# Optimization experiments

Measured on AMD Instinct MI355X. Metric: run time of the kernel, lower is better.

Reference implementation:

```python
import jax, jax.numpy as jnp
import numpy as np

H = 256
EDGE_DIM = 16
B, N = 8, 4096
E = 524288
EPS = 1e-5


def setup_inputs() -> dict:
    key = jax.random.key(0)
    ks = jax.random.split(key, 16)
    s = 0.02
    return {
        "h": jax.random.normal(ks[0], (B, N, H), dtype=jnp.float32),
        "edge_index": jax.random.randint(ks[1], (2, E), 0, B * N, dtype=jnp.int64),
        "edge_attr": jax.random.normal(ks[2], (E, EDGE_DIM), dtype=jnp.float32),
        "mask": jnp.ones((B, N), dtype=jnp.float32),
        # message_net params
        "W1": jax.random.normal(ks[3], (2 * H + EDGE_DIM, H), dtype=jnp.float32) * s,
        "b1": jnp.zeros((H,), dtype=jnp.float32),
        "W2": jax.random.normal(ks[4], (H, H), dtype=jnp.float32) * s,
        "b2": jnp.zeros((H,), dtype=jnp.float32),
        # update_net params
        "U1": jax.random.normal(ks[5], (2 * H, H), dtype=jnp.float32) * s,
        "c1": jnp.zeros((H,), dtype=jnp.float32),
        "U2": jax.random.normal(ks[6], (H, H), dtype=jnp.float32) * s,
        "c2": jnp.zeros((H,), dtype=jnp.float32),
        # LayerNorm params
        "gamma": jnp.ones((H,), dtype=jnp.float32),
        "beta": jnp.zeros((H,), dtype=jnp.float32),
    }


def reference(h, edge_index, edge_attr, mask, W1, b1, W2, b2, U1, c1, U2, c2, gamma, beta):
    batch, n_nodes, hid = h.shape
    h_flat = h.reshape(-1, hid)                       # (B*N, H)
    src, dst = edge_index[0], edge_index[1]
    # gather -> message MLP
    msg_in = jnp.concatenate([h_flat[src], h_flat[dst], edge_attr], axis=-1)  # (E, 2H+16)
    messages = jax.nn.silu(msg_in @ W1 + b1) @ W2 + b2                        # (E, H)
    # scatter-add aggregation by destination node
    aggr = jax.ops.segment_sum(messages, dst, num_segments=batch * n_nodes)   # (B*N, H)
    # update MLP + residual (dropout = identity in eval mode)
    upd_in = jnp.concatenate([h_flat, aggr], axis=-1)                         # (B*N, 2H)
    h_new = h_flat + (jax.nn.silu(upd_in @ U1 + c1) @ U2 + c2)
    # LayerNorm over last dim
    mu = jnp.mean(h_new, axis=-1, keepdims=True)
    var = jnp.mean(jnp.square(h_new - mu), axis=-1, keepdims=True)
    h_new = (h_new - mu) * jax.lax.rsqrt(var + EPS) * gamma + beta
    return h_new.reshape(batch, n_nodes, hid) * mask[..., None]
```

## Files before the change

kernel.cpp:

```cpp
#include <hip/hip_runtime.h>

#define H_DIM 256
#define E_NUM 524288
#define NN    32768
#define K2    512
#define K2S   520
#define SAS   264
#define XS    264

typedef unsigned short u16;
typedef unsigned int   u32;
typedef __attribute__((ext_vector_type(8))) short s16x8;
typedef __attribute__((ext_vector_type(4))) float f32x4;
typedef __attribute__((ext_vector_type(2))) float f32x2;
typedef __attribute__((ext_vector_type(4))) unsigned short u16x4;

__device__ __forceinline__ u16 f2b(float x) {
    u32 u = __float_as_uint(x);
    u32 r = (u + 0x7FFFu + ((u >> 16) & 1u)) >> 16;
    return (u16)r;
}
__device__ __forceinline__ float b2f(u16 v) {
    u32 u = ((u32)v) << 16;
    return __uint_as_float(u);
}
__device__ __forceinline__ float fsig(float x) {
    return __builtin_amdgcn_rcpf(1.f + __expf(-x));
}

__global__ __launch_bounds__(256) void k_prep_w(
    const float* __restrict__ W1, const float* __restrict__ W2,
    const float* __restrict__ U1, const float* __restrict__ U2,
    u16* __restrict__ WpqT, u16* __restrict__ W2T,
    u16* __restrict__ U1T, u16* __restrict__ U2T) {
    int idx = blockIdx.x * 256 + threadIdx.x;
    if (idx < 131072) {
        int c = idx >> 8, k = idx & 255;
        float v = (c < 256) ? W1[k * 256 + c] : W1[(256 + k) * 256 + (c - 256)];
        WpqT[idx] = f2b(v);
    } else if (idx < 196608) {
        int i = idx - 131072; int c = i >> 8, k = i & 255;
        W2T[i] = f2b(W2[k * 256 + c]);
    } else if (idx < 327680) {
        int i = idx - 196608; int c = i >> 9, k = i & 511;
        U1T[i] = f2b(U1[(size_t)k * 256 + c]);
    } else if (idx < 393216) {
        int i = idx - 327680; int c = i >> 8, k = i & 255;
        U2T[i] = f2b(U2[k * 256 + c]);
    }
}

__global__ __launch_bounds__(256) void k_hist(const int* __restrict__ eidx,
                                              int* __restrict__ cnt) {
    int i = blockIdx.x * 256 + threadIdx.x;
    if (i < E_NUM) atomicAdd(&cnt[eidx[E_NUM + i]], 1);
}

__global__ __launch_bounds__(256) void k_scan(const int* __restrict__ cnt,
                                              int* __restrict__ base,
                                              int* __restrict__ nxt) {
    __shared__ int wsum[4];
    const int t = threadIdx.x, lane = t & 63, w = t >> 6;
    const int st = t * 128;
    int s = 0;
#pragma unroll 8
    for (int i = 0; i < 128; ++i) s += cnt[st + i];
    int sc = s;
#pragma unroll
    for (int off = 1; off < 64; off <<= 1) {
        int v = __shfl_up(sc, off);
        if (lane >= off) sc += v;
    }
    if (lane == 63) wsum[w] = sc;
    __syncthreads();
    int woff = 0;
    for (int i = 0; i < w; ++i) woff += wsum[i];
    const int excl = woff + sc - s;
    if (t == 255) base[NN] = woff + sc;
    int off = excl;
    for (int i = 0; i < 128; ++i) {
        int v = cnt[st + i];
        base[st + i] = off;
        nxt[st + i] = off;
        off += v;
    }
}

__global__ __launch_bounds__(256) void k_scatter(const int* __restrict__ eidx,
                                                 int* __restrict__ nxt,
                                                 int* __restrict__ elist,
                                                 float* __restrict__ eas,
                                                 const float* __restrict__ ea) {
    int i = blockIdx.x * 256 + threadIdx.x;
    if (i < E_NUM) {
        int d = eidx[E_NUM + i];
        int p = atomicAdd(&nxt[d], 1);
        elist[p] = eidx[i];
        const float4* s = reinterpret_cast<const float4*>(ea + (size_t)i * 16);
        float4* o = reinterpret_cast<float4*>(eas + (size_t)p * 16);
        float4 v0 = s[0], v1 = s[1], v2 = s[2], v3 = s[3];
        o[0] = v0; o[1] = v1; o[2] = v2; o[3] = v3;
    }
}

__global__ __launch_bounds__(256, 2) void k_gemm_pq(
    const float* __restrict__ h, const u16* __restrict__ WpqT,
    u16* __restrict__ PQ) {
    __shared__ __align__(16) u16 sA[64 * SAS];
    const int t = threadIdx.x;
    const int n0 = blockIdx.x * 64;
    {
        const int r = t >> 2, g = t & 3;
        const float* hrow = h + (size_t)(n0 + r) * 256;
        u16* rowp = sA + r * SAS;
#pragma unroll
        for (int j = 0; j < 8; ++j) {
            const int c = g + 4 * j;
            float4 v0 = *reinterpret_cast<const float4*>(hrow + c * 8);
            float4 v1 = *reinterpret_cast<const float4*>(hrow + c * 8 + 4);
            s16x8 o;
            o[0] = (short)f2b(v0.x); o[1] = (short)f2b(v0.y);
            o[2] = (short)f2b(v0.z); o[3] = (short)f2b(v0.w);
            o[4] = (short)f2b(v1.x); o[5] = (short)f2b(v1.y);
            o[6] = (short)f2b(v1.z); o[7] = (short)f2b(v1.w);
            *reinterpret_cast<s16x8*>(rowp + c * 8) = o;
        }
    }
    __syncthreads();
    const int lane = t & 63, wv = t >> 6;
    const int l15 = lane & 15, l4 = lane >> 4;
    const int colBase = wv * 64 + l15;
    const f32x4 z4 = {0.f, 0.f, 0.f, 0.f};

    for (int q = 0; q < 2; ++q) {
        f32x4 acc[4][4];
#pragma unroll
        for (int m = 0; m < 4; ++m)
#pragma unroll
            for (int n = 0; n < 4; ++n) acc[m][n] = z4;
        const u16* Bb = WpqT + (size_t)(q * 256 + colBase) * 256 + l4 * 8;
        for (int kk = 0; kk < 8; ++kk) {
            s16x8 a[4], b[4];
#pragma unroll
            for (int m = 0; m < 4; ++m)
                a[m] = *reinterpret_cast<const s16x8*>(sA + (m * 16 + l15) * SAS + kk * 32 + l4 * 8);
#pragma unroll
            for (int n = 0; n < 4; ++n)
                b[n] = *reinterpret_cast<const s16x8*>(Bb + (size_t)n * 16 * 256 + kk * 32);
#pragma unroll
            for (int m = 0; m < 4; ++m)
#pragma unroll
                for (int n = 0; n < 4; ++n)
                    acc[m][n] = __builtin_amdgcn_mfma_f32_16x16x32_bf16(a[m], b[n], acc[m][n], 0, 0, 0);
        }
#pragma unroll
        for (int m = 0; m < 4; ++m)
#pragma unroll
            for (int j = 0; j < 4; ++j) {
                const int row = n0 + m * 16 + l4 * 4 + j;
                u16* op = PQ + (size_t)row * 512 + q * 256 + colBase;
#pragma unroll
                for (int n = 0; n < 4; ++n) op[n * 16] = f2b(acc[m][n][j]);
            }
    }
}


#define LDEA(S0, S1, S2, S3, k) do {                                        \
    const float* _ep = eas + (size_t)(eBeg + cb + min((k), m - 1)) * 16;    \
    S0 = *reinterpret_cast<const float4*>(_ep);                             \
    S1 = *reinterpret_cast<const float4*>(_ep + 4);                         \
    S2 = *reinterpret_cast<const float4*>(_ep + 8);                         \
    S3 = *reinterpret_cast<const float4*>(_ep + 12);                        \
} while (0)

__global__ __launch_bounds__(256, 4) void k_aggr(
    const u16* __restrict__ PQ, const int* __restrict__ elist,
    const int* __restrict__ base, const float* __restrict__ eas,
    const float* __restrict__ W1, const float* __restrict__ b1,
    u16* __restrict__ Sb) {
    const int t = threadIdx.x, lane = t & 63, wv = t >> 6;
    const int c0 = lane * 4;
    f32x2 WrL[16], WrH[16];
#pragma unroll
    for (int k = 0; k < 16; ++k) {
        float4 w = *reinterpret_cast<const float4*>(W1 + (size_t)(512 + k) * 256 + c0);
        WrL[k] = f32x2{w.x, w.y};
        WrH[k] = f32x2{w.z, w.w};
    }
    const float4 b1v = *reinterpret_cast<const float4*>(b1 + c0);

    const int d = __builtin_amdgcn_readfirstlane(blockIdx.x * 4 + wv);
    f32x2 qbL = {b1v.x, b1v.y}, qbH = {b1v.z, b1v.w};
    {
        u16x4 qv = *reinterpret_cast<const u16x4*>(PQ + (size_t)d * 512 + 256 + c0);
        qbL[0] += b2f(qv.x); qbL[1] += b2f(qv.y);
        qbH[0] += b2f(qv.z); qbH[1] += b2f(qv.w);
    }
    const int eBeg = __builtin_amdgcn_readfirstlane(base[d]);
    const int nAll = __builtin_amdgcn_readfirstlane(base[d + 1]) - eBeg;
    f32x2 accL = {0.f, 0.f}, accH = {0.f, 0.f};

    for (int cb = 0; cb < nAll; cb += 64) {
        const int m = min(64, nAll - cb);
        const int eeX = elist[eBeg + cb + min(lane, m - 1)];

        auto gather = [&](int idx) -> u16x4 {
            const int s = __builtin_amdgcn_readlane(eeX, idx);
            return *reinterpret_cast<const u16x4*>(PQ + (size_t)s * 512 + c0);
        };
        auto edge_compute = [&](const u16x4& pc, const float4& E0, const float4& E1,
                                const float4& E2, const float4& E3) {
            f32x2 xL = qbL, xH = qbH;
            xL[0] += b2f(pc.x); xL[1] += b2f(pc.y);
            xH[0] += b2f(pc.z); xH[1] += b2f(pc.w);
            xL = xL + WrL[0]  * E0.x; xH = xH + WrH[0]  * E0.x;
            xL = xL + WrL[1]  * E0.y; xH = xH + WrH[1]  * E0.y;
            xL = xL + WrL[2]  * E0.z; xH = xH + WrH[2]  * E0.z;
            xL = xL + WrL[3]  * E0.w; xH = xH + WrH[3]  * E0.w;
            xL = xL + WrL[4]  * E1.x; xH = xH + WrH[4]  * E1.x;
            xL = xL + WrL[5]  * E1.y; xH = xH + WrH[5]  * E1.y;
            xL = xL + WrL[6]  * E1.z; xH = xH + WrH[6]  * E1.z;
            xL = xL + WrL[7]  * E1.w; xH = xH + WrH[7]  * E1.w;
            xL = xL + WrL[8]  * E2.x; xH = xH + WrH[8]  * E2.x;
            xL = xL + WrL[9]  * E2.y; xH = xH + WrH[9]  * E2.y;
            xL = xL + WrL[10] * E2.z; xH = xH + WrH[10] * E2.z;
            xL = xL + WrL[11] * E2.w; xH = xH + WrH[11] * E2.w;
            xL = xL + WrL[12] * E3.x; xH = xH + WrH[12] * E3.x;
            xL = xL + WrL[13] * E3.y; xH = xH + WrH[13] * E3.y;
            xL = xL + WrL[14] * E3.z; xH = xH + WrH[14] * E3.z;
            xL = xL + WrL[15] * E3.w; xH = xH + WrH[15] * E3.w;
            accL[0] += xL[0] * fsig(xL[0]);
            accL[1] += xL[1] * fsig(xL[1]);
            accH[0] += xH[0] * fsig(xH[0]);
            accH[1] += xH[1] * fsig(xH[1]);
        };

        u16x4 p0 = gather(0), p1 = gather(1), p2 = gather(2), p3 = gather(3);
        float4 A0, A1, A2, A3, B0, B1, B2, B3;
        LDEA(A0, A1, A2, A3, 0);
        LDEA(B0, B1, B2, B3, 1);
        int kb = 0;
        for (; kb + 4 <= m; kb += 4) {
            edge_compute(p0, A0, A1, A2, A3);
            LDEA(A0, A1, A2, A3, kb + 2);
            p0 = gather(min(kb + 4, 63));
            edge_compute(p1, B0, B1, B2, B3);
            LDEA(B0, B1, B2, B3, kb + 3);
            p1 = gather(min(kb + 5, 63));
            edge_compute(p2, A0, A1, A2, A3);
            LDEA(A0, A1, A2, A3, kb + 4);
            p2 = gather(min(kb + 6, 63));
            edge_compute(p3, B0, B1, B2, B3);
            LDEA(B0, B1, B2, B3, kb + 5);
            p3 = gather(min(kb + 7, 63));
        }
        if (kb + 0 < m) edge_compute(p0, A0, A1, A2, A3);
        if (kb + 1 < m) edge_compute(p1, B0, B1, B2, B3);
        if (kb + 2 < m) {
            LDEA(A0, A1, A2, A3, kb + 2);
            edge_compute(p2, A0, A1, A2, A3);
        }
    }
    u16x4 o;
    o.x = f2b(accL[0]); o.y = f2b(accL[1]);
    o.z = f2b(accH[0]); o.w = f2b(accH[1]);
    *reinterpret_cast<u16x4*>(Sb + (size_t)d * 256 + c0) = o;
}

__global__ __launch_bounds__(256, 2) void k_post(
    const float* __restrict__ h, const u16* __restrict__ Sb,
    const u16* __restrict__ W2T, const int* __restrict__ base,
    const float* __restrict__ b2,
    const u16* __restrict__ U1T, const u16* __restrict__ U2T,
    const float* __restrict__ c1, const float* __restrict__ c2,
    const float* __restrict__ gamma, const float* __restrict__ beta,
    const float* __restrict__ mask,
    float* __restrict__ out) {
    __shared__ __align__(16) char smemraw[64 * XS * 4];
    u16* sA = reinterpret_cast<u16*>(smemraw);
    const int t  = threadIdx.x;
    const int n0 = blockIdx.x * 64;

    {
        const int r = t >> 2, g = t & 3;
        const int node = n0 + r;
        const float* hrow = h + (size_t)node * H_DIM;
        const u16* srow = Sb + (size_t)node * H_DIM;
        u16* rowp = sA + r * K2S;
#pragma unroll
        for (int j = 0; j < 16; ++j) {
            const int c = g + 4 * j;
            if (c < 32) {
                float4 v0 = *reinterpret_cast<const float4*>(hrow + c * 8);
                float4 v1 = *reinterpret_cast<const float4*>(hrow + c * 8 + 4);
                s16x8 o;
                o[0] = (short)f2b(v0.x); o[1] = (short)f2b(v0.y);
                o[2] = (short)f2b(v0.z); o[3] = (short)f2b(v0.w);
                o[4] = (short)f2b(v1.x); o[5] = (short)f2b(v1.y);
                o[6] = (short)f2b(v1.z); o[7] = (short)f2b(v1.w);
                *reinterpret_cast<s16x8*>(rowp + c * 8) = o;
            } else {
                const int cc = c - 32;
                *reinterpret_cast<s16x8*>(rowp + 256 + cc * 8) =
                    *reinterpret_cast<const s16x8*>(srow + cc * 8);
            }
        }
    }
    __syncthreads();

    const int lane = t & 63, wv = t >> 6;
    const int l15 = lane & 15, l4 = lane >> 4;
    const int colBase = wv * 64 + l15;
    const f32x4 z4 = {0.f, 0.f, 0.f, 0.f};

    f32x4 acc[4][4];
#pragma unroll
    for (int m = 0; m < 4; ++m)
#pragma unroll
        for (int n = 0; n < 4; ++n) acc[m][n] = z4;

    {
        const u16* Bb = W2T + (size_t)colBase * 256 + l4 * 8;
        for (int kk = 0; kk < 8; ++kk) {
            s16x8 a[4], b[4];
#pragma unroll
            for (int m = 0; m < 4; ++m)
                a[m] = *reinterpret_cast<const s16x8*>(sA + (m * 16 + l15) * K2S + 256 + kk * 32 + l4 * 8);
#pragma unroll
            for (int n = 0; n < 4; ++n)
                b[n] = *reinterpret_cast<const s16x8*>(Bb + (size_t)n * 16 * 256 + kk * 32);
#pragma unroll
            for (int m = 0; m < 4; ++m)
#pragma unroll
                for (int n = 0; n < 4; ++n)
                    acc[m][n] = __builtin_amdgcn_mfma_f32_16x16x32_bf16(a[m], b[n], acc[m][n], 0, 0, 0);
        }
    }
    __syncthreads();

    {
        float b2v[4];
#pragma unroll
        for (int n = 0; n < 4; ++n) b2v[n] = b2[colBase + n * 16];
#pragma unroll
        for (int m = 0; m < 4; ++m)
#pragma unroll
            for (int j = 0; j < 4; ++j) {
                const int row = m * 16 + l4 * 4 + j;
                const float dv = (float)(base[n0 + row + 1] - base[n0 + row]);
#pragma unroll
                for (int n = 0; n < 4; ++n)
                    sA[row * K2S + 256 + colBase + n * 16] = f2b(acc[m][n][j] + dv * b2v[n]);
            }
    }
    __syncthreads();

#pragma unroll
    for (int m = 0; m < 4; ++m)
#pragma unroll
        for (int n = 0; n < 4; ++n) acc[m][n] = z4;
    {
        const u16* Bb = U1T + (size_t)colBase * K2 + l4 * 8;
        for (int kk = 0; kk < 16; ++kk) {
            s16x8 a[4], b[4];
#pragma unroll
            for (int m = 0; m < 4; ++m)
                a[m] = *reinterpret_cast<const s16x8*>(sA + (m * 16 + l15) * K2S + kk * 32 + l4 * 8);
#pragma unroll
            for (int n = 0; n < 4; ++n)
                b[n] = *reinterpret_cast<const s16x8*>(Bb + (size_t)n * 16 * K2 + kk * 32);
#pragma unroll
            for (int m = 0; m < 4; ++m)
#pragma unroll
                for (int n = 0; n < 4; ++n)
                    acc[m][n] = __builtin_amdgcn_mfma_f32_16x16x32_bf16(a[m], b[n], acc[m][n], 0, 0, 0);
        }
    }
    __syncthreads();

    {
        u16* sX = reinterpret_cast<u16*>(smemraw);
        float c1v[4];
#pragma unroll
        for (int n = 0; n < 4; ++n) c1v[n] = c1[colBase + n * 16];
#pragma unroll
        for (int m = 0; m < 4; ++m)
#pragma unroll
            for (int n = 0; n < 4; ++n)
#pragma unroll
                for (int j = 0; j < 4; ++j) {
                    float x = acc[m][n][j] + c1v[n];
                    float s = x * fsig(x);
                    sX[(m * 16 + l4 * 4 + j) * XS + colBase + n * 16] = f2b(s);
                }
    }
    __syncthreads();

#pragma unroll
    for (int m = 0; m < 4; ++m)
#pragma unroll
        for (int n = 0; n < 4; ++n) acc[m][n] = z4;
    {
        const u16* sX = reinterpret_cast<u16*>(smemraw);
        const u16* Bb = U2T + (size_t)colBase * H_DIM + l4 * 8;
        for (int kk = 0; kk < 8; ++kk) {
            s16x8 a[4], b[4];
#pragma unroll
            for (int m = 0; m < 4; ++m)
                a[m] = *reinterpret_cast<const s16x8*>(sX + (m * 16 + l15) * XS + kk * 32 + l4 * 8);
#pragma unroll
            for (int n = 0; n < 4; ++n)
                b[n] = *reinterpret_cast<const s16x8*>(Bb + (size_t)n * 16 * H_DIM + kk * 32);
#pragma unroll
            for (int m = 0; m < 4; ++m)
#pragma unroll
                for (int n = 0; n < 4; ++n)
                    acc[m][n] = __builtin_amdgcn_mfma_f32_16x16x32_bf16(a[m], b[n], acc[m][n], 0, 0, 0);
        }
    }
    __syncthreads();

    {
        float* sF = reinterpret_cast<float*>(smemraw);
        float c2v[4];
#pragma unroll
        for (int n = 0; n < 4; ++n) c2v[n] = c2[colBase + n * 16];
#pragma unroll
        for (int m = 0; m < 4; ++m)
#pragma unroll
            for (int n = 0; n < 4; ++n)
#pragma unroll
                for (int j = 0; j < 4; ++j) {
                    const int row = m * 16 + l4 * 4 + j;
                    const float hv = h[(size_t)(n0 + row) * H_DIM + colBase + n * 16];
                    sF[row * XS + colBase + n * 16] = acc[m][n][j] + c2v[n] + hv;
                }
    }
    __syncthreads();

    {
        const float* sF = reinterpret_cast<const float*>(smemraw);
        const int rr = t >> 2, p = t & 3;
        const float* rowf = sF + rr * XS + p * 64;
        float s1 = 0.f, s2 = 0.f;
#pragma unroll
        for (int i = 0; i < 64; ++i) { float v = rowf[i]; s1 += v; s2 += v * v; }
        s1 += __shfl_xor(s1, 1); s1 += __shfl_xor(s1, 2);
        s2 += __shfl_xor(s2, 1); s2 += __shfl_xor(s2, 2);
        const float mu   = s1 * (1.f / 256.f);
        const float var  = s2 * (1.f / 256.f) - mu * mu;
        const float rstd = rsqrtf(var + 1e-5f);
        const int node = n0 + rr;
        const float mk = mask[node];
        float* op = out + (size_t)node * H_DIM + p * 64;
        const float* gp = gamma + p * 64;
        const float* bp = beta + p * 64;
#pragma unroll
        for (int i = 0; i < 64; i += 4) {
            float4 x  = *reinterpret_cast<const float4*>(rowf + i);
            float4 g4 = *reinterpret_cast<const float4*>(gp + i);
            float4 b4 = *reinterpret_cast<const float4*>(bp + i);
            float4 o;
            o.x = (((x.x - mu) * rstd) * g4.x + b4.x) * mk;
            o.y = (((x.y - mu) * rstd) * g4.y + b4.y) * mk;
            o.z = (((x.z - mu) * rstd) * g4.z + b4.z) * mk;
            o.w = (((x.w - mu) * rstd) * g4.w + b4.w) * mk;
            *reinterpret_cast<float4*>(op + i) = o;
        }
    }
}

#define OFF_PQ     0ull
#define OFF_SB     33554432ull
#define OFF_EAS    50331648ull
#define OFF_WPQT   83886080ull
#define OFF_W2T    84148224ull
#define OFF_U1T    84279296ull
#define OFF_U2T    84541440ull
#define OFF_CNT    84672512ull
#define OFF_BASE   84803584ull
#define OFF_NEXT   84934912ull
#define OFF_ELIST  85065984ull

extern "C" void kernel_launch(void* const* d_in, const int* in_sizes, int n_in,
                              void* d_out, int out_size, void* d_ws, size_t ws_size,
                              hipStream_t stream) {
    const float* h     = (const float*)d_in[0];
    const int*   eidx  = (const int*)d_in[1];
    const float* ea    = (const float*)d_in[2];
    const float* mask  = (const float*)d_in[3];
    const float* W1    = (const float*)d_in[4];
    const float* b1    = (const float*)d_in[5];
    const float* W2    = (const float*)d_in[6];
    const float* b2    = (const float*)d_in[7];
    const float* U1    = (const float*)d_in[8];
    const float* c1    = (const float*)d_in[9];
    const float* U2    = (const float*)d_in[10];
    const float* c2    = (const float*)d_in[11];
    const float* gamma = (const float*)d_in[12];
    const float* beta  = (const float*)d_in[13];
    float* out = (float*)d_out;
    char*  ws  = (char*)d_ws;

    u16*   PQ    = (u16*)(ws + OFF_PQ);
    u16*   Sb    = (u16*)(ws + OFF_SB);
    float* eas   = (float*)(ws + OFF_EAS);
    u16*   WpqT  = (u16*)(ws + OFF_WPQT);
    u16*   W2T   = (u16*)(ws + OFF_W2T);
    u16*   U1T   = (u16*)(ws + OFF_U1T);
    u16*   U2T   = (u16*)(ws + OFF_U2T);
    int*   cnt   = (int*)(ws + OFF_CNT);
    int*   base  = (int*)(ws + OFF_BASE);
    int*   nxt   = (int*)(ws + OFF_NEXT);
    int*   elist = (int*)(ws + OFF_ELIST);

    hipMemsetAsync(cnt, 0, (size_t)NN * sizeof(int), stream);

    k_prep_w<<<1536, 256, 0, stream>>>(W1, W2, U1, U2, WpqT, W2T, U1T, U2T);
    k_hist<<<E_NUM / 256, 256, 0, stream>>>(eidx, cnt);
    k_scan<<<1, 256, 0, stream>>>(cnt, base, nxt);
    k_scatter<<<E_NUM / 256, 256, 0, stream>>>(eidx, nxt, elist, eas, ea);
    k_gemm_pq<<<NN / 64, 256, 0, stream>>>(h, WpqT, PQ);
    k_aggr<<<NN / 4, 256, 0, stream>>>(PQ, elist, base, eas, W1, b1, Sb);
    k_post<<<NN / 64, 256, 0, stream>>>(h, Sb, W2T, base, b2, U1T, U2T,
                                        c1, c2, gamma, beta, mask, out);
}
```

Measured before the change: 281.8 us.

## Parallelize aggregation over edges with MFMA edge-attr projection and atomic segment sums

The aggregation kernel is restructured from one wavefront per destination node to fixed 16-edge chunks per wavefront over the destination-sorted edge list. The edge-attribute projection moves from per-lane scalar FMAs to a bf16 MFMA on an LDS tile, and edge attributes are stored as bf16. Per-destination runs are reduced in registers and flushed with float atomics into a zeroed fp32 buffer, which k_post now converts to bf16. This targets load imbalance from varying node degrees and the FMA-heavy per-edge work. It adds a large memset, atomic traffic and extra dlist and Q gathers per edge.

```diff
diff --git a/kernel.cpp b/kernel.cpp
--- a/kernel.cpp
+++ b/kernel.cpp
@@ -7,12 +7,12 @@
 #define K2S   520
 #define SAS   264
 #define XS    264
+#define RS    264
 
 typedef unsigned short u16;
 typedef unsigned int   u32;
 typedef __attribute__((ext_vector_type(8))) short s16x8;
 typedef __attribute__((ext_vector_type(4))) float f32x4;
-typedef __attribute__((ext_vector_type(2))) float f32x2;
 typedef __attribute__((ext_vector_type(4))) unsigned short u16x4;
 
 __device__ __forceinline__ u16 f2b(float x) {
@@ -32,7 +32,8 @@
     const float* __restrict__ W1, const float* __restrict__ W2,
     const float* __restrict__ U1, const float* __restrict__ U2,
     u16* __restrict__ WpqT, u16* __restrict__ W2T,
-    u16* __restrict__ U1T, u16* __restrict__ U2T) {
+    u16* __restrict__ U1T, u16* __restrict__ U2T,
+    u16* __restrict__ W1CT) {
     int idx = blockIdx.x * 256 + threadIdx.x;
     if (idx < 131072) {
         int c = idx >> 8, k = idx & 255;
@@ -47,6 +48,9 @@
     } else if (idx < 393216) {
         int i = idx - 327680; int c = i >> 8, k = i & 255;
         U2T[i] = f2b(U2[k * 256 + c]);
+    } else if (idx < 401408) {
+        int i = idx - 393216; int c = i >> 5, k = i & 31;
+        W1CT[i] = (k < 16) ? f2b(W1[(size_t)(512 + k) * 256 + c]) : (u16)0;
     }
 }
 
@@ -89,17 +93,28 @@
 __global__ __launch_bounds__(256) void k_scatter(const int* __restrict__ eidx,
                                                  int* __restrict__ nxt,
                                                  int* __restrict__ elist,
-                                                 float* __restrict__ eas,
+                                                 int* __restrict__ dlist,
+                                                 u16* __restrict__ easb,
                                                  const float* __restrict__ ea) {
     int i = blockIdx.x * 256 + threadIdx.x;
     if (i < E_NUM) {
         int d = eidx[E_NUM + i];
         int p = atomicAdd(&nxt[d], 1);
         elist[p] = eidx[i];
-        const float4* s = reinterpret_cast<const float4*>(ea + (size_t)i * 16);
-        float4* o = reinterpret_cast<float4*>(eas + (size_t)p * 16);
-        float4 v0 = s[0], v1 = s[1], v2 = s[2], v3 = s[3];
-        o[0] = v0; o[1] = v1; o[2] = v2; o[3] = v3;
+        dlist[p] = d;
+        const float4* s4 = reinterpret_cast<const float4*>(ea + (size_t)i * 16);
+        float4 a0 = s4[0], a1 = s4[1], a2 = s4[2], a3 = s4[3];
+        s16x8 o0, o1;
+        o0[0] = (short)f2b(a0.x); o0[1] = (short)f2b(a0.y);
+        o0[2] = (short)f2b(a0.z); o0[3] = (short)f2b(a0.w);
+        o0[4] = (short)f2b(a1.x); o0[5] = (short)f2b(a1.y);
+        o0[6] = (short)f2b(a1.z); o0[7] = (short)f2b(a1.w);
+        o1[0] = (short)f2b(a2.x); o1[1] = (short)f2b(a2.y);
+        o1[2] = (short)f2b(a2.z); o1[3] = (short)f2b(a2.w);
+        o1[4] = (short)f2b(a3.x); o1[5] = (short)f2b(a3.y);
+        o1[6] = (short)f2b(a3.z); o1[7] = (short)f2b(a3.w);
+        s16x8* o = reinterpret_cast<s16x8*>(easb + (size_t)p * 16);
+        o[0] = o0; o[1] = o1;
     }
 }
 
@@ -165,111 +180,109 @@
     }
 }
 
-
-#define LDEA(S0, S1, S2, S3, k) do {                                        \
-    const float* _ep = eas + (size_t)(eBeg + cb + min((k), m - 1)) * 16;    \
-    S0 = *reinterpret_cast<const float4*>(_ep);                             \
-    S1 = *reinterpret_cast<const float4*>(_ep + 4);                         \
-    S2 = *reinterpret_cast<const float4*>(_ep + 8);                         \
-    S3 = *reinterpret_cast<const float4*>(_ep + 12);                        \
-} while (0)
-
 __global__ __launch_bounds__(256, 4) void k_aggr(
     const u16* __restrict__ PQ, const int* __restrict__ elist,
-    const int* __restrict__ base, const float* __restrict__ eas,
-    const float* __restrict__ W1, const float* __restrict__ b1,
-    u16* __restrict__ Sb) {
+    const int* __restrict__ dlist, const u16* __restrict__ easb,
+    const u16* __restrict__ W1CT, const float* __restrict__ b1,
+    float* __restrict__ S) {
+    __shared__ __align__(16) u16 sEA[64 * 32];
+    __shared__ __align__(16) u16 sR[64 * RS];
     const int t = threadIdx.x, lane = t & 63, wv = t >> 6;
+    const int l15 = lane & 15, l4 = lane >> 4;
+    const int p0 = blockIdx.x * 64;
+
+    {
+        const int r = t >> 2, g = t & 3;
+        s16x8 v = s16x8{0, 0, 0, 0, 0, 0, 0, 0};
+        if (g < 2) v = *reinterpret_cast<const s16x8*>(easb + (size_t)(p0 + r) * 16 + g * 8);
+        *reinterpret_cast<s16x8*>(sEA + r * 32 + g * 8) = v;
+    }
+    __syncthreads();
+
+    {
+        const int colBase = wv * 64 + l15;
+        float b1v[4];
+#pragma unroll
+        for (int n = 0; n < 4; ++n) b1v[n] = b1[colBase + n * 16];
+        const f32x4 z4 = {0.f, 0.f, 0.f, 0.f};
+        f32x4 acc[4][4];
+#pragma unroll
+        for (int m = 0; m < 4; ++m)
+#pragma unroll
+            for (int n = 0; n < 4; ++n) acc[m][n] = z4;
+        s16x8 a[4], b[4];
+#pragma unroll
+        for (int m = 0; m < 4; ++m)
+            a[m] = *reinterpret_cast<const s16x8*>(sEA + (m * 16 + l15) * 32 + l4 * 8);
+#pragma unroll
+        for (int n = 0; n < 4; ++n)
+            b[n] = *reinterpret_cast<const s16x8*>(W1CT + (size_t)(colBase + n * 16) * 32 + l4 * 8);
+#pragma unroll
+        for (int m = 0; m < 4; ++m)
+#pragma unroll
+            for (int n = 0; n < 4; ++n)
+                acc[m][n] = __builtin_amdgcn_mfma_f32_16x16x32_bf16(a[m], b[n], acc[m][n], 0, 0, 0);
+#pragma unroll
+        for (int m = 0; m < 4; ++m)
+#pragma unroll
+            for (int n = 0; n < 4; ++n)
+#pragma unroll
+                for (int j = 0; j < 4; ++j)
+                    sR[(m * 16 + l4 * 4 + j) * RS + colBase + n * 16] =
+                        f2b(acc[m][n][j] + b1v[n]);
+    }
+    __syncthreads();
+
     const int c0 = lane * 4;
-    f32x2 WrL[16], WrH[16];
-#pragma unroll
-    for (int k = 0; k < 16; ++k) {
-        float4 w = *reinterpret_cast<const float4*>(W1 + (size_t)(512 + k) * 256 + c0);
-        WrL[k] = f32x2{w.x, w.y};
-        WrH[k] = f32x2{w.z, w.w};
-    }
-    const float4 b1v = *reinterpret_cast<const float4*>(b1 + c0);
-
-    const int d = __builtin_amdgcn_readfirstlane(blockIdx.x * 4 + wv);
-    f32x2 qbL = {b1v.x, b1v.y}, qbH = {b1v.z, b1v.w};
-    {
-        u16x4 qv = *reinterpret_cast<const u16x4*>(PQ + (size_t)d * 512 + 256 + c0);
-        qbL[0] += b2f(qv.x); qbL[1] += b2f(qv.y);
-        qbH[0] += b2f(qv.z); qbH[1] += b2f(qv.w);
-    }
-    const int eBeg = __builtin_amdgcn_readfirstlane(base[d]);
-    const int nAll = __builtin_amdgcn_readfirstlane(base[d + 1]) - eBeg;
-    f32x2 accL = {0.f, 0.f}, accH = {0.f, 0.f};
-
-    for (int cb = 0; cb < nAll; cb += 64) {
-        const int m = min(64, nAll - cb);
-        const int eeX = elist[eBeg + cb + min(lane, m - 1)];
-
-        auto gather = [&](int idx) -> u16x4 {
-            const int s = __builtin_amdgcn_readlane(eeX, idx);
-            return *reinterpret_cast<const u16x4*>(PQ + (size_t)s * 512 + c0);
-        };
-        auto edge_compute = [&](const u16x4& pc, const float4& E0, const float4& E1,
-                                const float4& E2, const float4& E3) {
-            f32x2 xL = qbL, xH = qbH;
-            xL[0] += b2f(pc.x); xL[1] += b2f(pc.y);
-            xH[0] += b2f(pc.z); xH[1] += b2f(pc.w);
-            xL = xL + WrL[0]  * E0.x; xH = xH + WrH[0]  * E0.x;
-            xL = xL + WrL[1]  * E0.y; xH = xH + WrH[1]  * E0.y;
-            xL = xL + WrL[2]  * E0.z; xH = xH + WrH[2]  * E0.z;
-            xL = xL + WrL[3]  * E0.w; xH = xH + WrH[3]  * E0.w;
-            xL = xL + WrL[4]  * E1.x; xH = xH + WrH[4]  * E1.x;
-            xL = xL + WrL[5]  * E1.y; xH = xH + WrH[5]  * E1.y;
-            xL = xL + WrL[6]  * E1.z; xH = xH + WrH[6]  * E1.z;
-            xL = xL + WrL[7]  * E1.w; xH = xH + WrH[7]  * E1.w;
-            xL = xL + WrL[8]  * E2.x; xH = xH + WrH[8]  * E2.x;
-            xL = xL + WrL[9]  * E2.y; xH = xH + WrH[9]  * E2.y;
-            xL = xL + WrL[10] * E2.z; xH = xH + WrH[10] * E2.z;
-            xL = xL + WrL[11] * E2.w; xH = xH + WrH[11] * E2.w;
-            xL = xL + WrL[12] * E3.x; xH = xH + WrH[12] * E3.x;
-            xL = xL + WrL[13] * E3.y; xH = xH + WrH[13] * E3.y;
-            xL = xL + WrL[14] * E3.z; xH = xH + WrH[14] * E3.z;
-            xL = xL + WrL[15] * E3.w; xH = xH + WrH[15] * E3.w;
-            accL[0] += xL[0] * fsig(xL[0]);
-            accL[1] += xL[1] * fsig(xL[1]);
-            accH[0] += xH[0] * fsig(xH[0]);
-            accH[1] += xH[1] * fsig(xH[1]);
-        };
-
-        u16x4 p0 = gather(0), p1 = gather(1), p2 = gather(2), p3 = gather(3);
-        float4 A0, A1, A2, A3, B0, B1, B2, B3;
-        LDEA(A0, A1, A2, A3, 0);
-        LDEA(B0, B1, B2, B3, 1);
-        int kb = 0;
-        for (; kb + 4 <= m; kb += 4) {
-            edge_compute(p0, A0, A1, A2, A3);
-            LDEA(A0, A1, A2, A3, kb + 2);
-            p0 = gather(min(kb + 4, 63));
-            edge_compute(p1, B0, B1, B2, B3);
-            LDEA(B0, B1, B2, B3, kb + 3);
-            p1 = gather(min(kb + 5, 63));
-            edge_compute(p2, A0, A1, A2, A3);
-            LDEA(A0, A1, A2, A3, kb + 4);
-            p2 = gather(min(kb + 6, 63));
-            edge_compute(p3, B0, B1, B2, B3);
-            LDEA(B0, B1, B2, B3, kb + 5);
-            p3 = gather(min(kb + 7, 63));
-        }
-        if (kb + 0 < m) edge_compute(p0, A0, A1, A2, A3);
-        if (kb + 1 < m) edge_compute(p1, B0, B1, B2, B3);
-        if (kb + 2 < m) {
-            LDEA(A0, A1, A2, A3, kb + 2);
-            edge_compute(p2, A0, A1, A2, A3);
-        }
-    }
-    u16x4 o;
-    o.x = f2b(accL[0]); o.y = f2b(accL[1]);
-    o.z = f2b(accH[0]); o.w = f2b(accH[1]);
-    *reinterpret_cast<u16x4*>(Sb + (size_t)d * 256 + c0) = o;
+    const int idx0 = __builtin_amdgcn_readfirstlane(p0 + wv * 16);
+
+    auto gathP = [&](int j) -> u16x4 {
+        const int sv = elist[idx0 + min(j, 15)];
+        return *reinterpret_cast<const u16x4*>(PQ + (size_t)sv * 512 + c0);
+    };
+    auto gathQ = [&](int j) -> u16x4 {
+        const int dv = dlist[idx0 + min(j, 15)];
+        return *reinterpret_cast<const u16x4*>(PQ + (size_t)dv * 512 + 256 + c0);
+    };
+
+    f32x4 acc3 = {0.f, 0.f, 0.f, 0.f};
+    int dcur = dlist[idx0];
+
+    auto step = [&](int i, const u16x4& pc, const u16x4& qc) {
+        const u16x4 rv = *reinterpret_cast<const u16x4*>(
+            sR + (size_t)(wv * 16 + i) * RS + c0);
+        float x0 = b2f(pc.x) + b2f(qc.x) + b2f(rv.x);
+        float x1 = b2f(pc.y) + b2f(qc.y) + b2f(rv.y);
+        float x2 = b2f(pc.z) + b2f(qc.z) + b2f(rv.z);
+        float x3 = b2f(pc.w) + b2f(qc.w) + b2f(rv.w);
+        acc3[0] += x0 * fsig(x0);
+        acc3[1] += x1 * fsig(x1);
+        acc3[2] += x2 * fsig(x2);
+        acc3[3] += x3 * fsig(x3);
+        const int dnext = (i < 15) ? dlist[idx0 + i + 1] : -1;
+        if (dnext != dcur) {
+            float* Sp = S + (size_t)dcur * 256 + c0;
+            atomicAdd(Sp + 0, acc3[0]);
+            atomicAdd(Sp + 1, acc3[1]);
+            atomicAdd(Sp + 2, acc3[2]);
+            atomicAdd(Sp + 3, acc3[3]);
+            acc3 = f32x4{0.f, 0.f, 0.f, 0.f};
+            dcur = dnext;
+        }
+    };
+
+    u16x4 P0 = gathP(0), P1 = gathP(1), P2 = gathP(2), P3 = gathP(3);
+    u16x4 Q0 = gathQ(0), Q1 = gathQ(1), Q2 = gathQ(2), Q3 = gathQ(3);
+    for (int kb = 0; kb < 16; kb += 4) {
+        step(kb + 0, P0, Q0); P0 = gathP(kb + 4); Q0 = gathQ(kb + 4);
+        step(kb + 1, P1, Q1); P1 = gathP(kb + 5); Q1 = gathQ(kb + 5);
+        step(kb + 2, P2, Q2); P2 = gathP(kb + 6); Q2 = gathQ(kb + 6);
+        step(kb + 3, P3, Q3); P3 = gathP(kb + 7); Q3 = gathQ(kb + 7);
+    }
 }
 
 __global__ __launch_bounds__(256, 2) void k_post(
-    const float* __restrict__ h, const u16* __restrict__ Sb,
+    const float* __restrict__ h, const float* __restrict__ S,
     const u16* __restrict__ W2T, const int* __restrict__ base,
     const float* __restrict__ b2,
     const u16* __restrict__ U1T, const u16* __restrict__ U2T,
@@ -286,25 +299,21 @@
         const int r = t >> 2, g = t & 3;
         const int node = n0 + r;
         const float* hrow = h + (size_t)node * H_DIM;
-        const u16* srow = Sb + (size_t)node * H_DIM;
+        const float* srow = S + (size_t)node * H_DIM;
         u16* rowp = sA + r * K2S;
 #pragma unroll
         for (int j = 0; j < 16; ++j) {
             const int c = g + 4 * j;
-            if (c < 32) {
-                float4 v0 = *reinterpret_cast<const float4*>(hrow + c * 8);
-                float4 v1 = *reinterpret_cast<const float4*>(hrow + c * 8 + 4);
-                s16x8 o;
-                o[0] = (short)f2b(v0.x); o[1] = (short)f2b(v0.y);
-                o[2] = (short)f2b(v0.z); o[3] = (short)f2b(v0.w);
-                o[4] = (short)f2b(v1.x); o[5] = (short)f2b(v1.y);
-                o[6] = (short)f2b(v1.z); o[7] = (short)f2b(v1.w);
-                *reinterpret_cast<s16x8*>(rowp + c * 8) = o;
-            } else {
-                const int cc = c - 32;
-                *reinterpret_cast<s16x8*>(rowp + 256 + cc * 8) =
-                    *reinterpret_cast<const s16x8*>(srow + cc * 8);
-            }
+            const float* src = (c < 32) ? (hrow + c * 8) : (srow + (c - 32) * 8);
+            float4 v0 = *reinterpret_cast<const float4*>(src);
+            float4 v1 = *reinterpret_cast<const float4*>(src + 4);
+            s16x8 o;
+            o[0] = (short)f2b(v0.x); o[1] = (short)f2b(v0.y);
+            o[2] = (short)f2b(v0.z); o[3] = (short)f2b(v0.w);
+            o[4] = (short)f2b(v1.x); o[5] = (short)f2b(v1.y);
+            o[6] = (short)f2b(v1.z); o[7] = (short)f2b(v1.w);
+            const int dstc = (c < 32) ? c : (c - 32);
+            *reinterpret_cast<s16x8*>(rowp + ((c < 32) ? 0 : 256) + dstc * 8) = o;
         }
     }
     __syncthreads();
@@ -471,17 +480,19 @@
     }
 }
 
-#define OFF_PQ     0ull
-#define OFF_SB     33554432ull
-#define OFF_EAS    50331648ull
-#define OFF_WPQT   83886080ull
-#define OFF_W2T    84148224ull
-#define OFF_U1T    84279296ull
-#define OFF_U2T    84541440ull
-#define OFF_CNT    84672512ull
-#define OFF_BASE   84803584ull
-#define OFF_NEXT   84934912ull
-#define OFF_ELIST  85065984ull
+#define OFF_S      0ull
+#define OFF_PQ     33554432ull
+#define OFF_EASB   67108864ull
+#define OFF_W1CT   83886080ull
+#define OFF_WPQT   83902464ull
+#define OFF_W2T    84164608ull
+#define OFF_U1T    84295680ull
+#define OFF_U2T    84557824ull
+#define OFF_CNT    84688896ull
+#define OFF_BASE   84819968ull
+#define OFF_NEXT   84951552ull
+#define OFF_ELIST  85082624ull
+#define OFF_DLIST  87179776ull
 
 extern "C" void kernel_launch(void* const* d_in, const int* in_sizes, int n_in,
                               void* d_out, int out_size, void* d_ws, size_t ws_size,
@@ -503,9 +514,10 @@
     float* out = (float*)d_out;
     char*  ws  = (char*)d_ws;
 
+    float* S     = (float*)(ws + OFF_S);
     u16*   PQ    = (u16*)(ws + OFF_PQ);
-    u16*   Sb    = (u16*)(ws + OFF_SB);
-    float* eas   = (float*)(ws + OFF_EAS);
+    u16*   easb  = (u16*)(ws + OFF_EASB);
+    u16*   W1CT  = (u16*)(ws + OFF_W1CT);
     u16*   WpqT  = (u16*)(ws + OFF_WPQT);
     u16*   W2T   = (u16*)(ws + OFF_W2T);
     u16*   U1T   = (u16*)(ws + OFF_U1T);
@@ -514,15 +526,17 @@
     int*   base  = (int*)(ws + OFF_BASE);
     int*   nxt   = (int*)(ws + OFF_NEXT);
     int*   elist = (int*)(ws + OFF_ELIST);
-
+    int*   dlist = (int*)(ws + OFF_DLIST);
+
+    hipMemsetAsync(S, 0, (size_t)NN * H_DIM * sizeof(float), stream);
     hipMemsetAsync(cnt, 0, (size_t)NN * sizeof(int), stream);
 
-    k_prep_w<<<1536, 256, 0, stream>>>(W1, W2, U1, U2, WpqT, W2T, U1T, U2T);
+    k_prep_w<<<1568, 256, 0, stream>>>(W1, W2, U1, U2, WpqT, W2T, U1T, U2T, W1CT);
     k_hist<<<E_NUM / 256, 256, 0, stream>>>(eidx, cnt);
     k_scan<<<1, 256, 0, stream>>>(cnt, base, nxt);
-    k_scatter<<<E_NUM / 256, 256, 0, stream>>>(eidx, nxt, elist, eas, ea);
+    k_scatter<<<E_NUM / 256, 256, 0, stream>>>(eidx, nxt, elist, dlist, easb, ea);
     k_gemm_pq<<<NN / 64, 256, 0, stream>>>(h, WpqT, PQ);
-    k_aggr<<<NN / 4, 256, 0, stream>>>(PQ, elist, base, eas, W1, b1, Sb);
-    k_post<<<NN / 64, 256, 0, stream>>>(h, Sb, W2T, base, b2, U1T, U2T,
+    k_aggr<<<E_NUM / 64, 256, 0, stream>>>(PQ, elist, dlist, easb, W1CT, b1, S);
+    k_post<<<NN / 64, 256, 0, stream>>>(h, S, W2T, base, b2, U1T, U2T,
                                         c1, c2, gamma, beta, mask, out);
 }
```

New measurement: 422.7 us. +50.0%, slower.
